# Optimization experiments

Measured on AMD Instinct MI355X. Metric: run time of the kernel, lower is better.

## Reference

```python
import jax, jax.numpy as jnp
import numpy as np

H = 1024   # lstm hidden size
F = 512    # feature dim
P = 66     # pose dim
T_IN = 10
T_OUT = 25


def _glorot(key, shape):
    fan = shape[-1]
    return jax.random.normal(key, shape, dtype=jnp.float32) / np.sqrt(fan)


def setup_inputs() -> dict:
    key = jax.random.key(0)
    ks = jax.random.split(key, 24)
    B = 256
    inp = {
        'x': jax.random.normal(ks[0], (B, T_IN, P), dtype=jnp.float32),
        'z': jax.random.normal(ks[1], (B, T_IN, P), dtype=jnp.float32),
        'for_resid': jax.random.normal(ks[2], (B, T_OUT, P), dtype=jnp.float32),
        # ToFeature: Linear(66 -> 512)
        'tf_w': _glorot(ks[3], (F, P)), 'tf_b': jnp.zeros((F,), jnp.float32),
        # encoder LSTM(512 -> 1024)
        'enc_wih': _glorot(ks[4], (4 * H, F)), 'enc_whh': _glorot(ks[5], (4 * H, H)),
        'enc_bih': jnp.zeros((4 * H,), jnp.float32), 'enc_bhh': jnp.zeros((4 * H,), jnp.float32),
        # encoder_post LSTM(512 -> 1024)
        'encp_wih': _glorot(ks[6], (4 * H, F)), 'encp_whh': _glorot(ks[7], (4 * H, H)),
        'encp_bih': jnp.zeros((4 * H,), jnp.float32), 'encp_bhh': jnp.zeros((4 * H,), jnp.float32),
        # decoder cell LSTM(512 -> 1024)
        'dec_wih': _glorot(ks[8], (4 * H, F)), 'dec_whh': _glorot(ks[9], (4 * H, H)),
        'dec_bih': jnp.zeros((4 * H,), jnp.float32), 'dec_bhh': jnp.zeros((4 * H,), jnp.float32),
        # decoder lin: Linear(1024 -> 512)
        'lin_w': _glorot(ks[10], (F, H)), 'lin_b': jnp.zeros((F,), jnp.float32),
        # ToPose: Linear(1024 -> 66)
        'tp_w': _glorot(ks[11], (P, H)), 'tp_b': jnp.zeros((P,), jnp.float32),
    }
    return inp


def _lstm_step(h, c, xt, wih, whh, bih, bhh):
    gates = xt @ wih.T + bih + h @ whh.T + bhh  # (B, 4H)
    i, f, g, o = jnp.split(gates, 4, axis=-1)
    c_new = jax.nn.sigmoid(f) * c + jax.nn.sigmoid(i) * jnp.tanh(g)
    h_new = jax.nn.sigmoid(o) * jnp.tanh(c_new)
    return h_new, c_new


def _lstm_scan(xs, wih, whh, bih, bhh):
    # xs: (T, B, I)
    B = xs.shape[1]
    h0 = jnp.zeros((B, H), xs.dtype)
    c0 = jnp.zeros((B, H), xs.dtype)

    def step(carry, xt):
        h, c = carry
        h, c = _lstm_step(h, c, xt, wih, whh, bih, bhh)
        return (h, c), h

    (h_n, c_n), all_h = jax.lax.scan(step, (h0, c0), xs)
    return all_h, h_n, c_n


def reference(x, z, for_resid, tf_w, tf_b,
              enc_wih, enc_whh, enc_bih, enc_bhh,
              encp_wih, encp_whh, encp_bih, encp_bhh,
              dec_wih, dec_whh, dec_bih, dec_bhh,
              lin_w, lin_b, tp_w, tp_b):
    # ToFeature + permute to time-major (T, B, F)
    xf = jnp.transpose(x @ tf_w.T + tf_b, (1, 0, 2))
    zf = jnp.transpose(z @ tf_w.T + tf_b, (1, 0, 2))

    all_h, h_n, c_n = _lstm_scan(xf, enc_wih, enc_whh, enc_bih, enc_bhh)   # (10,B,H)
    all_hz, _, _ = _lstm_scan(zf, encp_wih, encp_whh, encp_bih, encp_bhh)  # (10,B,H)

    def dec_step(carry, _):
        h, c = carry                                   # (B,H), (B,H)
        cat_h = jnp.concatenate([all_h, h[None], all_hz], axis=0)  # (21,B,H)
        scores = jnp.einsum('bh,tbh->tb', c, cat_h)
        attw = jax.nn.softmax(scores, axis=0)
        atth = jnp.einsum('tb,tbh->bh', attw, cat_h)   # attention context -> LSTM h0
        inp = h @ lin_w.T + lin_b                      # (B,F)
        h_new, c_new = _lstm_step(atth, c, inp, dec_wih, dec_whh, dec_bih, dec_bhh)
        return (h_new, c_new), h_new

    _, dec_hs = jax.lax.scan(dec_step, (h_n, c_n), None, length=T_OUT)  # (25,B,H)
    out = jnp.transpose(dec_hs, (1, 0, 2))             # (B,25,H)
    o = out @ tp_w.T + tp_b                            # (B,25,66)
    return o + for_resid
```

## Files before the change

### kernel.cpp

```cpp
#include <hip/hip_runtime.h>
#include <hip/hip_bf16.h>
#include <hip/hip_cooperative_groups.h>

namespace cg = cooperative_groups;

#define DEV __device__ __forceinline__

typedef unsigned short u16;
typedef short bf16x8_t __attribute__((ext_vector_type(8)));
typedef float f32x4_t __attribute__((ext_vector_type(4)));

constexpr int NBLK = 256;
constexpr int NTHR = 512;
constexpr int NT_ALL = NBLK * NTHR;
constexpr size_t HSTRIDE = 256 * 1024;
constexpr int SMEM_BYTES = 98304;

struct Params {
  const float *x, *z, *resid, *tf_w, *tf_b;
  const float *e_wih, *e_whh, *e_bih, *e_bhh;
  const float *p_wih, *p_whh, *p_bih, *p_bhh;
  const float *d_wih, *d_whh, *d_bih, *d_bhh;
  const float *lin_w, *lin_b, *tp_w, *tp_b;
  u16 *Wenc, *Wencp, *Wdec, *wihP, *linT, *tpw;
  float *bias_e, *bias_ep, *bias_d, *bias_part;
  u16 *xf, *zf;
  u16 *he, *hp;
  u16 *hs;
  u16 *atth;
  float *c_pub;
  unsigned long long *px;
  unsigned *flag1;
  unsigned *bar;
  float *out;
};

DEV float b2f(u16 v) { unsigned u = ((unsigned)v) << 16; float f; __builtin_memcpy(&f, &u, 4); return f; }
DEV u16 f2b(float f) {
  unsigned u; __builtin_memcpy(&u, &f, 4);
  unsigned r = u + 0x7fffu + ((u >> 16) & 1u);
  return (u16)(r >> 16);
}
DEV unsigned pk2(float a, float b) { return (unsigned)f2b(a) | ((unsigned)f2b(b) << 16); }
DEV uint4 cvt8(const float* s) {
  float4 a = *(const float4*)s;
  float4 b = *(const float4*)(s + 4);
  uint4 r;
  r.x = pk2(a.x, a.y); r.y = pk2(a.z, a.w);
  r.z = pk2(b.x, b.y); r.w = pk2(b.z, b.w);
  return r;
}
DEV float sigm(float x) { return 1.0f / (1.0f + __expf(-x)); }
DEV f32x4_t fzero4() { f32x4_t v = {0.f, 0.f, 0.f, 0.f}; return v; }

DEV void gll16(const void* g, void* l) {
  __builtin_amdgcn_global_load_lds(
      (const __attribute__((address_space(1))) void*)g,
      (__attribute__((address_space(3))) void*)l, 16, 0, 0);
}

template <typename T> DEV void st_wt(T* p, T v) {
  __hip_atomic_store(p, v, __ATOMIC_RELAXED, __HIP_MEMORY_SCOPE_AGENT);
}
template <typename T> DEV T ld_byp(const T* p) {
  return __hip_atomic_load(p, __ATOMIC_RELAXED, __HIP_MEMORY_SCOPE_AGENT);
}

DEV void fullbar(unsigned* ctrs, int myidx, unsigned tgt, int tid) {
  asm volatile("s_waitcnt vmcnt(0)" ::: "memory");
  __syncthreads();
  if (tid == 0) atomicAdd(&ctrs[myidx * 16], 1u);
  if (tid < 8) { while (ld_byp(&ctrs[tid * 16]) < tgt) __builtin_amdgcn_s_sleep(2); }
  __syncthreads();
}
DEV void gbar(unsigned* ctrs, int cbase, int myidx, unsigned tgt, int tid) {
  asm volatile("s_waitcnt vmcnt(0)" ::: "memory");
  __syncthreads();
  if (tid == 0) atomicAdd(&ctrs[(cbase + myidx) * 16], 1u);
  if (tid < 4) { while (ld_byp(&ctrs[(cbase + tid) * 16]) < tgt) __builtin_amdgcn_s_sleep(2); }
  __syncthreads();
}
DEV void lanebar(unsigned* ctrs, int cbase, unsigned tgt, int j, int tid) {
  asm volatile("s_waitcnt vmcnt(0)" ::: "memory");
  __syncthreads();
  if (tid == 0) atomicAdd(&ctrs[(cbase + (j & 1)) * 16], 1u);
  if (tid < 2) { while (ld_byp(&ctrs[(cbase + tid) * 16]) < tgt) __builtin_amdgcn_s_sleep(2); }
  __syncthreads();
}

template <int PM>
DEV void gemm64(const u16* __restrict__ xa, int ldx, int xcols,
                const u16* __restrict__ ha, int ldh,
                const u16* __restrict__ wsrc, int ldw, int K,
                int m0, int n0, int tid, char* sm, f32x4_t acc[4]) {
  char* lA = sm;
  char* lB = sm + 32768;
  const int NK = K >> 6;
  const int row = tid >> 3;
  const int usw = ((tid & 7) ^ (row & 7)) * 8;
  const int wv = tid >> 6;
  char* laD = lA + (wv << 10);
  char* lbD = lB + (wv << 10);
  const u16* aX = xa + (size_t)(m0 + row) * ldx + usw;
  const u16* aH = ha + (size_t)(m0 + row) * ldh + usw - xcols;
  const u16* bW0 = wsrc + (size_t)(n0 + row) * ldw + usw;
  const u16* bW1 = bW0 + (size_t)64 * ldw;

  auto sA = [&](int ks) {
    const int k0 = ks << 6;
    const u16* g = (k0 < xcols) ? (aX + k0) : (aH + k0);
    gll16(g, laD + (((ks + 2) & 3) << 13));
  };
  auto sB = [&](int ks) {
    const int k0 = ks << 6;
    const int so = ((ks + 2) & 3) << 14;
    gll16(bW0 + k0, lbD + so);
    gll16(bW1 + k0, lbD + so + 8192);
  };

  const int l = tid & 63, l15 = l & 15, lhi = l >> 4;
  const int wr = wv >> 2, wc = wv & 3;
  const int rA0 = wr * 32 + l15, rA1 = rA0 + 16;
  const int nB0 = wc * 32 + l15, nB1 = nB0 + 16;
  const int a00 = rA0 * 128 + ((lhi ^ (rA0 & 7)) << 4);
  const int a01 = rA0 * 128 + (((lhi + 4) ^ (rA0 & 7)) << 4);
  const int a10 = rA1 * 128 + ((lhi ^ (rA1 & 7)) << 4);
  const int a11 = rA1 * 128 + (((lhi + 4) ^ (rA1 & 7)) << 4);
  const int b00 = nB0 * 128 + ((lhi ^ (nB0 & 7)) << 4);
  const int b01 = nB0 * 128 + (((lhi + 4) ^ (nB0 & 7)) << 4);
  const int b10 = nB1 * 128 + ((lhi ^ (nB1 & 7)) << 4);
  const int b11 = nB1 * 128 + (((lhi + 4) ^ (nB1 & 7)) << 4);

  if (PM == 0) { sA(0); sB(0); sA(1); sB(1); }
  if (PM == 2) { sA(0); sA(1); }

#pragma unroll 1
  for (int ks = 0; ks < NK; ++ks) {
    if (ks + 2 < NK) { sA(ks + 2); sB(ks + 2); }
    if (PM == 2 && ks == 0)  asm volatile("s_waitcnt vmcnt(4)" ::: "memory");
    else if (ks + 2 < NK)    asm volatile("s_waitcnt vmcnt(6)" ::: "memory");
    else if (ks + 2 == NK)   asm volatile("s_waitcnt vmcnt(3)" ::: "memory");
    else                     asm volatile("s_waitcnt vmcnt(0)" ::: "memory");
    __builtin_amdgcn_s_barrier();
    const char* A  = lA + (((ks + 2) & 3) << 13);
    const char* Bq = lB + (((ks + 2) & 3) << 14);
#pragma unroll
    for (int kh = 0; kh < 2; ++kh) {
      bf16x8_t va0 = *(const bf16x8_t*)(A + (kh ? a01 : a00));
      bf16x8_t va1 = *(const bf16x8_t*)(A + (kh ? a11 : a10));
      bf16x8_t vb0 = *(const bf16x8_t*)(Bq + (kh ? b01 : b00));
      bf16x8_t vb1 = *(const bf16x8_t*)(Bq + (kh ? b11 : b10));
      acc[0] = __builtin_amdgcn_mfma_f32_16x16x32_bf16(va0, vb0, acc[0], 0, 0, 0);
      acc[1] = __builtin_amdgcn_mfma_f32_16x16x32_bf16(va0, vb1, acc[1], 0, 0, 0);
      acc[2] = __builtin_amdgcn_mfma_f32_16x16x32_bf16(va1, vb0, acc[2], 0, 0, 0);
      acc[3] = __builtin_amdgcn_mfma_f32_16x16x32_bf16(va1, vb1, acc[3], 0, 0, 0);
    }
  }
  asm volatile("s_waitcnt lgkmcnt(0)" ::: "memory");
  __builtin_amdgcn_s_barrier();
}

DEV void preA(const u16* src, int lds_, int m0, int tid, char* sm, int ks) {
  const int row = tid >> 3, usw = ((tid & 7) ^ (row & 7)) * 8, wv = tid >> 6;
  gll16(src + (size_t)(m0 + row) * lds_ + (ks << 6) + usw,
        sm + (wv << 10) + (((ks + 2) & 3) << 13));
}
DEV void preB(const u16* w, int ldw, int n0, int tid, char* sm, int ks) {
  const int row = tid >> 3, usw = ((tid & 7) ^ (row & 7)) * 8, wv = tid >> 6;
  char* d = sm + 32768 + (wv << 10) + (((ks + 2) & 3) << 14);
  gll16(w + (size_t)(n0 + row) * ldw + (ks << 6) + usw, d);
  gll16(w + (size_t)(n0 + 64 + row) * ldw + (ks << 6) + usw, d + 8192);
}

DEV void lstm_ep(const f32x4_t acc[4], int tid, char* sm,
                 const float* __restrict__ bias, float cc[4],
                 const float* __restrict__ cinit,
                 u16* __restrict__ hw, float* __restrict__ cpub,
                 int m0, int n0) {
  float* gl = (float*)sm;
  const int l = tid & 63, l15 = l & 15, lhi = l >> 4;
  const int wv = tid >> 6, wr = wv >> 2, wc = wv & 3;
#pragma unroll
  for (int mf = 0; mf < 2; ++mf)
#pragma unroll
    for (int nf = 0; nf < 2; ++nf)
#pragma unroll
      for (int qq = 0; qq < 4; ++qq)
        gl[(wr * 32 + mf * 16 + lhi * 4 + qq) * 128 + wc * 32 + nf * 16 + l15] =
            acc[mf * 2 + nf][qq];
  __syncthreads();
#pragma unroll
  for (int it = 0; it < 4; ++it) {
    int idx = it * 512 + tid;
    int r = idx >> 5, jj = idx & 31;
    f32x4_t g4 = *(const f32x4_t*)(gl + r * 128 + jj * 4);
    f32x4_t b4 = *(const f32x4_t*)(bias + n0 + jj * 4);
    float ig = sigm(g4[0] + b4[0]);
    float fg = sigm(g4[1] + b4[1]);
    float g_ = tanhf(g4[2] + b4[2]);
    float og = sigm(g4[3] + b4[3]);
    size_t off = (size_t)(m0 + r) * 1024 + (n0 >> 2) + jj;
    float cold = cinit ? ld_byp(cinit + off) : cc[it];
    float cn = fg * cold + ig * g_;
    cc[it] = cn;
    float hn = og * tanhf(cn);
    st_wt(&hw[off], f2b(hn));
    if (cpub) st_wt(&cpub[off], cn);
  }
  __syncthreads();
}

DEV void wx_store(const f32x4_t acc[4], int tid, u16* __restrict__ Wdec,
                  int m0, int n0) {
  const int l = tid & 63, l15 = l & 15, lhi = l >> 4;
  const int wv = tid >> 6, wr = wv >> 2, wc = wv & 3;
#pragma unroll
  for (int mf = 0; mf < 2; ++mf)
#pragma unroll
    for (int nf = 0; nf < 2; ++nf)
#pragma unroll
      for (int qq = 0; qq < 4; ++qq) {
        int r = m0 + wr * 32 + mf * 16 + lhi * 4 + qq;
        int c = n0 + wc * 32 + nf * 16 + l15;
        st_wt(&Wdec[(size_t)r * 2048 + c], f2b(acc[mf * 2 + nf][qq]));
      }
}

DEV void px_store(const f32x4_t acc[4], int tid, unsigned long long* base) {
#pragma unroll
  for (int i = 0; i < 8; ++i) {
    float lo = acc[i >> 1][(i & 1) * 2 + 0];
    float hi = acc[i >> 1][(i & 1) * 2 + 1];
    unsigned a_, b_; __builtin_memcpy(&a_, &lo, 4); __builtin_memcpy(&b_, &hi, 4);
    st_wt(base + (size_t)i * 512 + tid,
          (unsigned long long)a_ | ((unsigned long long)b_ << 32));
  }
}
DEV void px_merge(f32x4_t acc[4], int tid, const unsigned long long* base) {
#pragma unroll
  for (int i = 0; i < 8; ++i) {
    unsigned long long u = ld_byp(base + (size_t)i * 512 + tid);
    unsigned a_ = (unsigned)u, b_ = (unsigned)(u >> 32);
    float lo, hi; __builtin_memcpy(&lo, &a_, 4); __builtin_memcpy(&hi, &b_, 4);
    acc[i >> 1][(i & 1) * 2 + 0] += lo;
    acc[i >> 1][(i & 1) * 2 + 1] += hi;
  }
}

DEV void phase0_tf(const Params& p, int bid, int tid, char* sm) {
  float* xs = (float*)sm;
  float* zs = (float*)(sm + 2688);
  for (int g = tid; g < 660; g += NTHR) {
    int t = g / 66, qd = g - t * 66;
    xs[g] = p.x[((size_t)bid * 10 + t) * 66 + qd];
    zs[g] = p.z[((size_t)bid * 10 + t) * 66 + qd];
  }
  __syncthreads();
  const int n = tid;
  float accx[10], accz[10];
  float bn = p.tf_b[n];
#pragma unroll
  for (int t = 0; t < 10; ++t) { accx[t] = bn; accz[t] = bn; }
  const float* wrow = p.tf_w + (size_t)n * 66;
  for (int k = 0; k < 66; ++k) {
    float wk = wrow[k];
#pragma unroll
    for (int t = 0; t < 10; ++t) {
      accx[t] = fmaf(wk, xs[t * 66 + k], accx[t]);
      accz[t] = fmaf(wk, zs[t * 66 + k], accz[t]);
    }
  }
#pragma unroll
  for (int t = 0; t < 10; ++t) {
    p.xf[(size_t)t * 131072 + (size_t)bid * 512 + n] = f2b(accx[t]);
    p.zf[(size_t)t * 131072 + (size_t)bid * 512 + n] = f2b(accz[t]);
  }
  __syncthreads();
}

DEV void phase0a(const Params& p, int gtid) {
  for (int g = gtid; g < 786432; g += NT_ALL) {
    int row = g / 192;
    int u = g - row * 192;
    int k = u * 8;
    int nsrc = (row & 3) * 1024 + (row >> 2);
    const float* s1 = (k < 512) ? (p.e_wih + (size_t)nsrc * 512 + k)
                                : (p.e_whh + (size_t)nsrc * 1024 + (k - 512));
    ((uint4*)p.Wenc)[g] = cvt8(s1);
    const float* s2 = (k < 512) ? (p.p_wih + (size_t)nsrc * 512 + k)
                                : (p.p_whh + (size_t)nsrc * 1024 + (k - 512));
    ((uint4*)p.Wencp)[g] = cvt8(s2);
  }
  for (int g = gtid; g < 524288; g += NT_ALL) {
    int row = g >> 7, u = g & 127;
    int nsrc = (row & 3) * 1024 + (row >> 2);
    ((uint4*)p.Wdec)[row * 256 + 128 + u] = cvt8(p.d_whh + (size_t)nsrc * 1024 + u * 8);
  }
  for (int g = gtid; g < 262144; g += NT_ALL) {
    int row = g >> 6, u = g & 63;
    int nsrc = (row & 3) * 1024 + (row >> 2);
    ((uint4*)p.wihP)[g] = cvt8(p.d_wih + (size_t)nsrc * 512 + u * 8);
  }
  for (int g = gtid; g < 524288; g += NT_ALL) {
    int f = g >> 10, h = g & 1023;
    p.linT[(size_t)h * 512 + f] = f2b(p.lin_w[g]);
  }
  for (int g = gtid; g < 8448; g += NT_ALL)
    ((uint4*)p.tpw)[g] = cvt8(p.tp_w + g * 8);
  for (int g = gtid; g < 4096; g += NT_ALL) {
    int nsrc = (g & 3) * 1024 + (g >> 2);
    p.bias_e[g]  = p.e_bih[nsrc] + p.e_bhh[nsrc];
    p.bias_ep[g] = p.p_bih[nsrc] + p.p_bhh[nsrc];
  }
  for (int g = gtid; g < 32768; g += NT_ALL) {
    int cell = g >> 3, sub = g & 7;
    int nsrc = (cell & 3) * 1024 + (cell >> 2);
    const float* wr_ = p.d_wih + (size_t)nsrc * 512 + sub * 64;
    const float* lb = p.lin_b + sub * 64;
    float s = 0.f;
    for (int f = 0; f < 64; ++f) s += wr_[f] * lb[f];
    p.bias_part[g] = s;
  }
  uint4 zz; zz.x = zz.y = zz.z = zz.w = 0u;
  for (int g = gtid; g < 32768; g += NT_ALL) { ((uint4*)p.he)[g] = zz; ((uint4*)p.hp)[g] = zz; }
}

DEV void attention(const Params& p, const u16* hd_prev, const float* cpub,
                   u16* atth_s, int b, int tid, char* sm) {
  u16*   catl = (u16*)sm;
  float* cl   = (float*)(sm + 43008);
  float* sc   = (float*)(sm + 47104);
  for (int g = tid; g < 2688; g += NTHR) {
    int t = g >> 7, hu = g & 127;
    const u16* src;
    if (t < 10)       src = p.he + (size_t)(t + 1) * HSTRIDE;
    else if (t == 10) src = hd_prev;
    else              src = p.hp + (size_t)(t - 10) * HSTRIDE;
    ((uint4*)catl)[g] = *(const uint4*)(src + (size_t)b * 1024 + hu * 8);
  }
  for (int g = tid; g < 512; g += NTHR) {
    unsigned long long v = ld_byp(((const unsigned long long*)(cpub + (size_t)b * 1024)) + g);
    ((unsigned long long*)cl)[g] = v;
  }
  __syncthreads();
  const int wv = tid >> 6, l = tid & 63;
  for (int t = wv; t < 21; t += 8) {
    float s = 0.f;
    const u16* cr = catl + t * 1024;
    for (int hh = l; hh < 1024; hh += 64) s += cl[hh] * b2f(cr[hh]);
#pragma unroll
    for (int o = 32; o; o >>= 1) s += __shfl_down(s, o);
    if (l == 0) sc[t] = s;
  }
  __syncthreads();
  float m = -1e30f;
#pragma unroll
  for (int t = 0; t < 21; ++t) m = fmaxf(m, sc[t]);
  float e[21]; float den = 0.f;
#pragma unroll
  for (int t = 0; t < 21; ++t) { e[t] = __expf(sc[t] - m); den += e[t]; }
  float inv = 1.0f / den;
  const int h0 = tid * 2;
  float a0 = 0.f, a1 = 0.f;
#pragma unroll
  for (int t = 0; t < 21; ++t) {
    float w_ = e[t] * inv;
    unsigned v = *(const unsigned*)(catl + t * 1024 + h0);
    a0 += w_ * b2f((u16)(v & 0xffff));
    a1 += w_ * b2f((u16)(v >> 16));
  }
  st_wt(((unsigned*)(atth_s + (size_t)b * 1024)) + tid, pk2(a0, a1));
  __syncthreads();
}

DEV void finalproj(const Params& p, int b, int tid, char* sm) {
  u16* hl = (u16*)sm;
  for (int g = tid; g < 3200; g += NTHR) {
    int t = g >> 7, hu = g & 127;
    ((uint4*)hl)[g] = *(const uint4*)(p.hs + ((size_t)(t * 256 + b)) * 1024 + hu * 8);
  }
  __syncthreads();
  if (tid < 330) {
    int pcol = tid % 66, tg = tid / 66;
    float acc[5] = {0.f, 0.f, 0.f, 0.f, 0.f};
    const u16* wrow = p.tpw + (size_t)pcol * 1024;
    for (int hc = 0; hc < 128; ++hc) {
      uint4 wv4 = ((const uint4*)wrow)[hc];
      float wf[8];
      wf[0] = b2f(wv4.x & 0xffff); wf[1] = b2f(wv4.x >> 16);
      wf[2] = b2f(wv4.y & 0xffff); wf[3] = b2f(wv4.y >> 16);
      wf[4] = b2f(wv4.z & 0xffff); wf[5] = b2f(wv4.z >> 16);
      wf[6] = b2f(wv4.w & 0xffff); wf[7] = b2f(wv4.w >> 16);
#pragma unroll
      for (int r = 0; r < 5; ++r) {
        int t = tg * 5 + r;
        uint4 hv = ((const uint4*)(hl + t * 1024))[hc];
        float s;
        s  = wf[0] * b2f(hv.x & 0xffff) + wf[1] * b2f(hv.x >> 16);
        s += wf[2] * b2f(hv.y & 0xffff) + wf[3] * b2f(hv.y >> 16);
        s += wf[4] * b2f(hv.z & 0xffff) + wf[5] * b2f(hv.z >> 16);
        s += wf[6] * b2f(hv.w & 0xffff) + wf[7] * b2f(hv.w >> 16);
        acc[r] += s;
      }
    }
    float bb = p.tp_b[pcol];
#pragma unroll
    for (int r = 0; r < 5; ++r) {
      int t = tg * 5 + r;
      size_t o = (size_t)b * 1650 + (size_t)t * 66 + pcol;
      p.out[o] = acc[r] + bb + p.resid[o];
    }
  }
}

__global__ __launch_bounds__(NTHR) void model_kernel(Params p) {
  cg::grid_group gg = cg::this_grid();
  extern __shared__ __align__(16) char sm[];
  const int tid = threadIdx.x;
  const int bid = blockIdx.x;
  const int gtid = bid * NTHR + tid;

  phase0_tf(p, bid, tid, sm);
  phase0a(p, gtid);
  if (bid == 0) {
    if (tid < 24)  st_wt(&p.bar[tid * 16], 0u);
    if (tid < 128) st_wt(&p.flag1[tid * 16], 0u);
  }
  gg.sync();

  for (int g = gtid; g < 4096; g += NT_ALL) {
    int nsrc = (g & 3) * 1024 + (g >> 2);
    float s = p.d_bih[nsrc] + p.d_bhh[nsrc];
#pragma unroll
    for (int k8 = 0; k8 < 8; ++k8) s += p.bias_part[g * 8 + k8];
    st_wt(&p.bias_d[g], s);
  }
#pragma unroll 1
  for (int i = 0; i < 2; ++i) {
    int tt = bid * 2 + i;
    int m0w = (tt & 63) << 6;
    int n0w = (tt >> 6) << 7;
    f32x4_t acc[4] = {fzero4(), fzero4(), fzero4(), fzero4()};
    gemm64<0>(p.wihP, 512, 512, p.wihP, 512, p.linT, 512, 512, m0w, n0w, tid, sm, acc);
    wx_store(acc, tid, p.Wdec, m0w, n0w);
  }

  const int grp = bid >> 7;
  const int q = bid & 127;
  const int m0 = (q >> 5) << 6;
  const int n0 = (q & 31) << 7;
  const int cb = grp ? 12 : 8;
  const int cidx = q >> 5;

  const int lane = bid >> 6, j = bid & 63;
  const int m0d = lane << 6;
  const int role = j >> 5, jj = j & 31;
  const int n0d = jj << 7;
  const int tixd = lane * 32 + jj;

  const u16* xsrc = grp ? p.zf : p.xf;
  const u16* Wg   = grp ? p.Wencp : p.Wenc;
  u16* hbuf       = grp ? p.hp : p.he;
  const float* bias_g = grp ? p.bias_ep : p.bias_e;

  preA(xsrc, 512, m0, tid, sm, 0);
  preB(Wg, 1536, n0, tid, sm, 0);
  preA(xsrc, 512, m0, tid, sm, 1);
  preB(Wg, 1536, n0, tid, sm, 1);
  fullbar(p.bar, bid & 7, 1u * 32, tid);

  float cc[4] = {0.f, 0.f, 0.f, 0.f};

#pragma unroll 1
  for (int t = 0; t < 10; ++t) {
    f32x4_t acc[4] = {fzero4(), fzero4(), fzero4(), fzero4()};
    gemm64<1>(xsrc + (size_t)t * 131072, 512, 512, hbuf + (size_t)t * HSTRIDE, 1024,
              Wg, 1536, 1536, m0, n0, tid, sm, acc);
    lstm_ep(acc, tid, sm, bias_g, cc, (const float*)0,
            hbuf + (size_t)(t + 1) * HSTRIDE,
            (!grp && t == 9) ? p.c_pub : (float*)0, m0, n0);
    if (t < 9) {
      preA(xsrc + (size_t)(t + 1) * 131072, 512, m0, tid, sm, 0);
      preB(Wg, 1536, n0, tid, sm, 0);
      preA(xsrc + (size_t)(t + 1) * 131072, 512, m0, tid, sm, 1);
      preB(Wg, 1536, n0, tid, sm, 1);
    } else {
      const u16* wd = role ? (p.Wdec + 1024) : p.Wdec;
      preB(wd, 2048, n0d, tid, sm, 0);
      preB(wd, 2048, n0d, tid, sm, 1);
    }
    gbar(p.bar, cb, cidx, (unsigned)(t + 1) * 32, tid);
  }
  fullbar(p.bar, bid & 7, 2u * 32, tid);

  float cd[4] = {0.f, 0.f, 0.f, 0.f};
  unsigned long long* px0 = p.px + (size_t)tixd * 4096;
  unsigned long long* px1 = p.px + (size_t)(128 + tixd) * 4096;
#pragma unroll 1
  for (int s = 0; s < 25; ++s) {
    const u16* hd_prev = (s == 0) ? (p.he + (size_t)10 * HSTRIDE)
                                  : (p.hs + (size_t)(s - 1) * HSTRIDE);
    u16* atth_s = p.atth + (size_t)s * HSTRIDE;
    attention(p, hd_prev, p.c_pub + (size_t)(s & 1) * 262144, atth_s, bid, tid, sm);
    lanebar(p.bar, 16 + lane * 2, (unsigned)(2 * s + 1) * 32, j, tid);
    f32x4_t acc[4] = {fzero4(), fzero4(), fzero4(), fzero4()};
    unsigned long long* pxs = (s & 1) ? px1 : px0;
    if (role == 0) {
      gemm64<2>(hd_prev, 1024, 1024, hd_prev, 1024, p.Wdec, 2048, 1024,
                m0d, n0d, tid, sm, acc);
      px_store(acc, tid, pxs);
      asm volatile("s_waitcnt vmcnt(0)" ::: "memory");
      __syncthreads();
      if (tid == 0) st_wt(&p.flag1[tixd * 16], (unsigned)(s + 1));
      preB(p.Wdec, 2048, n0d, tid, sm, 0);
      preB(p.Wdec, 2048, n0d, tid, sm, 1);
    } else {
      gemm64<2>(atth_s, 1024, 1024, atth_s, 1024, p.Wdec + 1024, 2048, 1024,
                m0d, n0d, tid, sm, acc);
      if (tid == 0) {
        while (ld_byp(&p.flag1[tixd * 16]) < (unsigned)(s + 1)) __builtin_amdgcn_s_sleep(2);
      }
      __syncthreads();
      px_merge(acc, tid, pxs);
      lstm_ep(acc, tid, sm, p.bias_d, cd,
              (s == 0) ? p.c_pub : (const float*)0,
              p.hs + (size_t)s * HSTRIDE,
              p.c_pub + (size_t)((s + 1) & 1) * 262144, m0d, n0d);
      preB(p.Wdec + 1024, 2048, n0d, tid, sm, 0);
      preB(p.Wdec + 1024, 2048, n0d, tid, sm, 1);
    }
    lanebar(p.bar, 16 + lane * 2, (unsigned)(2 * s + 2) * 32, j, tid);
  }

  finalproj(p, bid, tid, sm);
}

extern "C" void kernel_launch(void* const* d_in, const int* in_sizes, int n_in,
                              void* d_out, int out_size, void* d_ws, size_t ws_size,
                              hipStream_t stream) {
  (void)in_sizes; (void)n_in; (void)out_size;
  Params P;
  P.x     = (const float*)d_in[0];
  P.z     = (const float*)d_in[1];
  P.resid = (const float*)d_in[2];
  P.tf_w  = (const float*)d_in[3];
  P.tf_b  = (const float*)d_in[4];
  P.e_wih = (const float*)d_in[5];
  P.e_whh = (const float*)d_in[6];
  P.e_bih = (const float*)d_in[7];
  P.e_bhh = (const float*)d_in[8];
  P.p_wih = (const float*)d_in[9];
  P.p_whh = (const float*)d_in[10];
  P.p_bih = (const float*)d_in[11];
  P.p_bhh = (const float*)d_in[12];
  P.d_wih = (const float*)d_in[13];
  P.d_whh = (const float*)d_in[14];
  P.d_bih = (const float*)d_in[15];
  P.d_bhh = (const float*)d_in[16];
  P.lin_w = (const float*)d_in[17];
  P.lin_b = (const float*)d_in[18];
  P.tp_w  = (const float*)d_in[19];
  P.tp_b  = (const float*)d_in[20];

  char* w = (char*)d_ws;
  size_t o = 0;
  auto take = [&](size_t bytes) { char* r = w + o; o = (o + bytes + 255) & ~(size_t)255; return r; };
  P.Wenc  = (u16*)take(4096ull * 1536 * 2);
  P.Wencp = (u16*)take(4096ull * 1536 * 2);
  P.Wdec  = (u16*)take(4096ull * 2048 * 2);
  P.wihP  = (u16*)take(4096ull * 512 * 2);
  P.linT  = (u16*)take(1024ull * 512 * 2);
  P.tpw   = (u16*)take(66ull * 1024 * 2);
  P.bias_e    = (float*)take(4096 * 4);
  P.bias_ep   = (float*)take(4096 * 4);
  P.bias_d    = (float*)take(4096 * 4);
  P.bias_part = (float*)take(32768 * 4);
  P.xf  = (u16*)take(10ull * 256 * 512 * 2);
  P.zf  = (u16*)take(10ull * 256 * 512 * 2);
  P.he  = (u16*)take(11ull * 256 * 1024 * 2);
  P.hp  = (u16*)take(11ull * 256 * 1024 * 2);
  P.hs  = (u16*)take(25ull * 256 * 1024 * 2);
  P.atth = (u16*)take(25ull * 256 * 1024 * 2);
  P.c_pub = (float*)take(2ull * 256 * 1024 * 4);
  P.px    = (unsigned long long*)take(2ull * 128 * 4096 * 8);
  P.flag1 = (unsigned*)take(128 * 64);
  P.bar   = (unsigned*)take(24 * 64);
  P.out = (float*)d_out;

  if (o > ws_size) return;

  hipFuncSetAttribute((const void*)model_kernel,
                      hipFuncAttributeMaxDynamicSharedMemorySize, SMEM_BYTES);

  void* args[] = { &P };
  hipLaunchCooperativeKernel((const void*)model_kernel, dim3(NBLK, 1, 1),
                             dim3(NTHR, 1, 1), args, SMEM_BYTES, stream);
}
```

Before: 905.8 us.

## Split decoder GEMM by N tiles instead of K halves, removing partial-sum exchange

Each decoder block used to compute half of the K reduction (h part or attention part) and swap partial sums through global memory with a flag handshake. Now each block computes a 64x64 output tile over the full K, running the h-part GEMM before the lane barrier and the attention part after it. This removes the px store/merge traffic and the flag spin-wait, and overlaps the h-part GEMM with waiting for attention. In exchange tiles are smaller (less MFMA reuse per load), lane barriers now count 8 counters instead of 2, and the attention shared-memory buffers are moved to avoid the new staging area.

```diff
diff --git a/kernel.cpp b/kernel.cpp
--- a/kernel.cpp
+++ b/kernel.cpp
@@ -29,8 +29,6 @@
   u16 *hs;
   u16 *atth;
   float *c_pub;
-  unsigned long long *px;
-  unsigned *flag1;
   unsigned *bar;
   float *out;
 };
@@ -66,10 +64,10 @@
   return __hip_atomic_load(p, __ATOMIC_RELAXED, __HIP_MEMORY_SCOPE_AGENT);
 }
 
-DEV void fullbar(unsigned* ctrs, int myidx, unsigned tgt, int tid) {
+DEV void fullbar(unsigned* ctrs, int bid, unsigned tgt, int tid) {
   asm volatile("s_waitcnt vmcnt(0)" ::: "memory");
   __syncthreads();
-  if (tid == 0) atomicAdd(&ctrs[myidx * 16], 1u);
+  if (tid == 0) atomicAdd(&ctrs[(bid & 7) * 16], 1u);
   if (tid < 8) { while (ld_byp(&ctrs[tid * 16]) < tgt) __builtin_amdgcn_s_sleep(2); }
   __syncthreads();
 }
@@ -80,19 +78,19 @@
   if (tid < 4) { while (ld_byp(&ctrs[(cbase + tid) * 16]) < tgt) __builtin_amdgcn_s_sleep(2); }
   __syncthreads();
 }
-DEV void lanebar(unsigned* ctrs, int cbase, unsigned tgt, int j, int tid) {
+DEV void lanebar8(unsigned* ctrs, int lane, int j, unsigned tgt, int tid) {
   asm volatile("s_waitcnt vmcnt(0)" ::: "memory");
   __syncthreads();
-  if (tid == 0) atomicAdd(&ctrs[(cbase + (j & 1)) * 16], 1u);
-  if (tid < 2) { while (ld_byp(&ctrs[(cbase + tid) * 16]) < tgt) __builtin_amdgcn_s_sleep(2); }
+  if (tid == 0) atomicAdd(&ctrs[(16 + lane * 8 + (j & 7)) * 16], 1u);
+  if (tid < 8) { while (ld_byp(&ctrs[(16 + lane * 8 + tid) * 16]) < tgt) __builtin_amdgcn_s_sleep(1); }
   __syncthreads();
 }
 
 template <int PM>
-DEV void gemm64(const u16* __restrict__ xa, int ldx, int xcols,
-                const u16* __restrict__ ha, int ldh,
-                const u16* __restrict__ wsrc, int ldw, int K,
-                int m0, int n0, int tid, char* sm, f32x4_t acc[4]) {
+DEV void gemm128(const u16* __restrict__ xa, int ldx, int xcols,
+                 const u16* __restrict__ ha, int ldh,
+                 const u16* __restrict__ wsrc, int ldw, int K,
+                 int m0, int n0, int tid, char* sm, f32x4_t acc[4]) {
   char* lA = sm;
   char* lB = sm + 32768;
   const int NK = K >> 6;
@@ -132,15 +130,13 @@
   const int b11 = nB1 * 128 + (((lhi + 4) ^ (nB1 & 7)) << 4);
 
   if (PM == 0) { sA(0); sB(0); sA(1); sB(1); }
-  if (PM == 2) { sA(0); sA(1); }
 
 #pragma unroll 1
   for (int ks = 0; ks < NK; ++ks) {
     if (ks + 2 < NK) { sA(ks + 2); sB(ks + 2); }
-    if (PM == 2 && ks == 0)  asm volatile("s_waitcnt vmcnt(4)" ::: "memory");
-    else if (ks + 2 < NK)    asm volatile("s_waitcnt vmcnt(6)" ::: "memory");
-    else if (ks + 2 == NK)   asm volatile("s_waitcnt vmcnt(3)" ::: "memory");
-    else                     asm volatile("s_waitcnt vmcnt(0)" ::: "memory");
+    if (ks + 2 < NK)        asm volatile("s_waitcnt vmcnt(6)" ::: "memory");
+    else if (ks + 2 == NK)  asm volatile("s_waitcnt vmcnt(3)" ::: "memory");
+    else                    asm volatile("s_waitcnt vmcnt(0)" ::: "memory");
     __builtin_amdgcn_s_barrier();
     const char* A  = lA + (((ks + 2) & 3) << 13);
     const char* Bq = lB + (((ks + 2) & 3) << 14);
@@ -160,23 +156,86 @@
   __builtin_amdgcn_s_barrier();
 }
 
-DEV void preA(const u16* src, int lds_, int m0, int tid, char* sm, int ks) {
+DEV void preA128(const u16* src, int lds_, int m0, int tid, char* sm, int ks) {
   const int row = tid >> 3, usw = ((tid & 7) ^ (row & 7)) * 8, wv = tid >> 6;
   gll16(src + (size_t)(m0 + row) * lds_ + (ks << 6) + usw,
         sm + (wv << 10) + (((ks + 2) & 3) << 13));
 }
-DEV void preB(const u16* w, int ldw, int n0, int tid, char* sm, int ks) {
+DEV void preB128(const u16* w, int ldw, int n0, int tid, char* sm, int ks) {
   const int row = tid >> 3, usw = ((tid & 7) ^ (row & 7)) * 8, wv = tid >> 6;
   char* d = sm + 32768 + (wv << 10) + (((ks + 2) & 3) << 14);
   gll16(w + (size_t)(n0 + row) * ldw + (ks << 6) + usw, d);
   gll16(w + (size_t)(n0 + 64 + row) * ldw + (ks << 6) + usw, d + 8192);
 }
 
-DEV void lstm_ep(const f32x4_t acc[4], int tid, char* sm,
-                 const float* __restrict__ bias, float cc[4],
-                 const float* __restrict__ cinit,
-                 u16* __restrict__ hw, float* __restrict__ cpub,
-                 int m0, int n0) {
+DEV void gemm64d(const u16* __restrict__ a, int lda,
+                 const u16* __restrict__ w, int ldw, int K,
+                 int m0, int n0, int tid, char* sm, f32x4_t acc[2]) {
+  char* lB = sm;
+  char* lA = sm + 32768;
+  const int NK = K >> 6;
+  const int row = tid >> 3, uu = tid & 7;
+  const int usw = uu ^ (row & 7);
+  const int wv = tid >> 6;
+  char* la_base = lA + (wv << 10);
+  char* lb_base = lB + (wv << 10);
+  const u16* aS = a + (size_t)(m0 + row) * lda + usw * 8;
+  const u16* bS = w + (size_t)(n0 + row) * ldw + usw * 8;
+
+  auto stageA = [&](int ks) { gll16(aS + (ks << 6), la_base + ((ks & 3) << 13)); };
+  auto stage  = [&](int ks) {
+    gll16(aS + (ks << 6), la_base + ((ks & 3) << 13));
+    gll16(bS + (ks << 6), lb_base + ((ks & 3) << 13));
+  };
+
+  const int l = tid & 63, l15 = l & 15, lhi = l >> 4;
+  const int wr = wv >> 1, wc = wv & 1;
+  const int rA = wr * 16 + l15;
+  const int aoff0 = rA * 128 + ((lhi ^ (rA & 7)) << 4);
+  const int aoff1 = rA * 128 + (((lhi + 4) ^ (rA & 7)) << 4);
+  const int nB0 = wc * 32 + l15, nB1 = nB0 + 16;
+  const int boff00 = nB0 * 128 + ((lhi ^ (nB0 & 7)) << 4);
+  const int boff01 = nB0 * 128 + (((lhi + 4) ^ (nB0 & 7)) << 4);
+  const int boff10 = nB1 * 128 + ((lhi ^ (nB1 & 7)) << 4);
+  const int boff11 = nB1 * 128 + (((lhi + 4) ^ (nB1 & 7)) << 4);
+
+  stageA(0); stageA(1);
+
+#pragma unroll 1
+  for (int ks = 0; ks < NK; ++ks) {
+    if (ks + 2 < NK) stage(ks + 2);
+    if (ks == 0)            asm volatile("s_waitcnt vmcnt(3)" ::: "memory");
+    else if (ks + 2 < NK)   asm volatile("s_waitcnt vmcnt(4)" ::: "memory");
+    else if (ks + 2 == NK)  asm volatile("s_waitcnt vmcnt(2)" ::: "memory");
+    else                    asm volatile("s_waitcnt vmcnt(0)" ::: "memory");
+    __builtin_amdgcn_s_barrier();
+    const char* A  = lA + ((ks & 3) << 13);
+    const char* Bb = lB + ((ks & 3) << 13);
+    bf16x8_t a0  = *(const bf16x8_t*)(A + aoff0);
+    bf16x8_t a1  = *(const bf16x8_t*)(A + aoff1);
+    bf16x8_t b00 = *(const bf16x8_t*)(Bb + boff00);
+    bf16x8_t b01 = *(const bf16x8_t*)(Bb + boff01);
+    bf16x8_t b10 = *(const bf16x8_t*)(Bb + boff10);
+    bf16x8_t b11 = *(const bf16x8_t*)(Bb + boff11);
+    acc[0] = __builtin_amdgcn_mfma_f32_16x16x32_bf16(a0, b00, acc[0], 0, 0, 0);
+    acc[0] = __builtin_amdgcn_mfma_f32_16x16x32_bf16(a1, b01, acc[0], 0, 0, 0);
+    acc[1] = __builtin_amdgcn_mfma_f32_16x16x32_bf16(a0, b10, acc[1], 0, 0, 0);
+    acc[1] = __builtin_amdgcn_mfma_f32_16x16x32_bf16(a1, b11, acc[1], 0, 0, 0);
+  }
+  asm volatile("s_waitcnt lgkmcnt(0)" ::: "memory");
+  __builtin_amdgcn_s_barrier();
+}
+
+DEV void preB64(const u16* w, int ldw, int n0, int tid, char* sm, int ks) {
+  const int row = tid >> 3, usw = (tid & 7) ^ (row & 7), wv = tid >> 6;
+  gll16(w + (size_t)(n0 + row) * ldw + (ks << 6) + usw * 8,
+        sm + (wv << 10) + ((ks & 3) << 13));
+}
+
+DEV void lstm_ep128(const f32x4_t acc[4], int tid, char* sm,
+                    const float* __restrict__ bias, float cc[4],
+                    u16* __restrict__ hw, float* __restrict__ cpub,
+                    int m0, int n0) {
   float* gl = (float*)sm;
   const int l = tid & 63, l15 = l & 15, lhi = l >> 4;
   const int wv = tid >> 6, wr = wv >> 2, wc = wv & 3;
@@ -194,6 +253,40 @@
     int idx = it * 512 + tid;
     int r = idx >> 5, jj = idx & 31;
     f32x4_t g4 = *(const f32x4_t*)(gl + r * 128 + jj * 4);
+    f32x4_t b4 = *(const f32x4_t*)(bias + n0 + jj * 4);
+    float ig = sigm(g4[0] + b4[0]);
+    float fg = sigm(g4[1] + b4[1]);
+    float g_ = tanhf(g4[2] + b4[2]);
+    float og = sigm(g4[3] + b4[3]);
+    float cn = fg * cc[it] + ig * g_;
+    cc[it] = cn;
+    float hn = og * tanhf(cn);
+    size_t off = (size_t)(m0 + r) * 1024 + (n0 >> 2) + jj;
+    st_wt(&hw[off], f2b(hn));
+    if (cpub) st_wt(&cpub[off], cn);
+  }
+  __syncthreads();
+}
+
+DEV void lstm_ep64(const f32x4_t acc[2], int tid, char* sm,
+                   const float* __restrict__ bias, float cc[2],
+                   const float* __restrict__ cinit,
+                   u16* __restrict__ hw, float* __restrict__ cpub,
+                   int m0, int n0) {
+  float* gl = (float*)(sm + 49152);
+  const int l = tid & 63, l15 = l & 15, lhi = l >> 4;
+  const int wv = tid >> 6, wr = wv >> 1, wc = wv & 1;
+#pragma unroll
+  for (int jf = 0; jf < 2; ++jf)
+#pragma unroll
+    for (int qq = 0; qq < 4; ++qq)
+      gl[(wr * 16 + lhi * 4 + qq) * 64 + wc * 32 + jf * 16 + l15] = acc[jf][qq];
+  __syncthreads();
+#pragma unroll
+  for (int it = 0; it < 2; ++it) {
+    int idx = it * 512 + tid;
+    int r = idx >> 4, jj = idx & 15;
+    f32x4_t g4 = *(const f32x4_t*)(gl + r * 64 + jj * 4);
     f32x4_t b4 = *(const f32x4_t*)(bias + n0 + jj * 4);
     float ig = sigm(g4[0] + b4[0]);
     float fg = sigm(g4[1] + b4[1]);
@@ -226,27 +319,6 @@
       }
 }
 
-DEV void px_store(const f32x4_t acc[4], int tid, unsigned long long* base) {
-#pragma unroll
-  for (int i = 0; i < 8; ++i) {
-    float lo = acc[i >> 1][(i & 1) * 2 + 0];
-    float hi = acc[i >> 1][(i & 1) * 2 + 1];
-    unsigned a_, b_; __builtin_memcpy(&a_, &lo, 4); __builtin_memcpy(&b_, &hi, 4);
-    st_wt(base + (size_t)i * 512 + tid,
-          (unsigned long long)a_ | ((unsigned long long)b_ << 32));
-  }
-}
-DEV void px_merge(f32x4_t acc[4], int tid, const unsigned long long* base) {
-#pragma unroll
-  for (int i = 0; i < 8; ++i) {
-    unsigned long long u = ld_byp(base + (size_t)i * 512 + tid);
-    unsigned a_ = (unsigned)u, b_ = (unsigned)(u >> 32);
-    float lo, hi; __builtin_memcpy(&lo, &a_, 4); __builtin_memcpy(&hi, &b_, 4);
-    acc[i >> 1][(i & 1) * 2 + 0] += lo;
-    acc[i >> 1][(i & 1) * 2 + 1] += hi;
-  }
-}
-
 DEV void phase0_tf(const Params& p, int bid, int tid, char* sm) {
   float* xs = (float*)sm;
   float* zs = (float*)(sm + 2688);
@@ -327,9 +399,9 @@
 
 DEV void attention(const Params& p, const u16* hd_prev, const float* cpub,
                    u16* atth_s, int b, int tid, char* sm) {
-  u16*   catl = (u16*)sm;
-  float* cl   = (float*)(sm + 43008);
-  float* sc   = (float*)(sm + 47104);
+  u16*   catl = (u16*)(sm + 16384);
+  float* cl   = (float*)(sm + 59392);
+  float* sc   = (float*)(sm + 63488);
   for (int g = tid; g < 2688; g += NTHR) {
     int t = g >> 7, hu = g & 127;
     const u16* src;
@@ -422,10 +494,7 @@
 
   phase0_tf(p, bid, tid, sm);
   phase0a(p, gtid);
-  if (bid == 0) {
-    if (tid < 24)  st_wt(&p.bar[tid * 16], 0u);
-    if (tid < 128) st_wt(&p.flag1[tid * 16], 0u);
-  }
+  if (bid == 0 && tid < 48) st_wt(&p.bar[tid * 16], 0u);
   gg.sync();
 
   for (int g = gtid; g < 4096; g += NT_ALL) {
@@ -435,101 +504,85 @@
     for (int k8 = 0; k8 < 8; ++k8) s += p.bias_part[g * 8 + k8];
     st_wt(&p.bias_d[g], s);
   }
+
 #pragma unroll 1
   for (int i = 0; i < 2; ++i) {
     int tt = bid * 2 + i;
     int m0w = (tt & 63) << 6;
     int n0w = (tt >> 6) << 7;
     f32x4_t acc[4] = {fzero4(), fzero4(), fzero4(), fzero4()};
-    gemm64<0>(p.wihP, 512, 512, p.wihP, 512, p.linT, 512, 512, m0w, n0w, tid, sm, acc);
+    gemm128<0>(p.wihP, 512, 512, p.wihP, 512, p.linT, 512, 512,
+               m0w, n0w, tid, sm, acc);
     wx_store(acc, tid, p.Wdec, m0w, n0w);
   }
 
   const int grp = bid >> 7;
   const int q = bid & 127;
-  const int m0 = (q >> 5) << 6;
-  const int n0 = (q & 31) << 7;
+  const int m0e = (q >> 5) << 6;
+  const int n0e = (q & 31) << 7;
   const int cb = grp ? 12 : 8;
   const int cidx = q >> 5;
 
   const int lane = bid >> 6, j = bid & 63;
   const int m0d = lane << 6;
-  const int role = j >> 5, jj = j & 31;
-  const int n0d = jj << 7;
-  const int tixd = lane * 32 + jj;
+  const int n0d = ((j & 7) * 8 + (j >> 3)) << 6;
 
   const u16* xsrc = grp ? p.zf : p.xf;
   const u16* Wg   = grp ? p.Wencp : p.Wenc;
   u16* hbuf       = grp ? p.hp : p.he;
   const float* bias_g = grp ? p.bias_ep : p.bias_e;
 
-  preA(xsrc, 512, m0, tid, sm, 0);
-  preB(Wg, 1536, n0, tid, sm, 0);
-  preA(xsrc, 512, m0, tid, sm, 1);
-  preB(Wg, 1536, n0, tid, sm, 1);
-  fullbar(p.bar, bid & 7, 1u * 32, tid);
+  preA128(xsrc, 512, m0e, tid, sm, 0);
+  preB128(Wg, 1536, n0e, tid, sm, 0);
+  preA128(xsrc, 512, m0e, tid, sm, 1);
+  preB128(Wg, 1536, n0e, tid, sm, 1);
+  fullbar(p.bar, bid, 32u, tid);
 
   float cc[4] = {0.f, 0.f, 0.f, 0.f};
 
 #pragma unroll 1
   for (int t = 0; t < 10; ++t) {
     f32x4_t acc[4] = {fzero4(), fzero4(), fzero4(), fzero4()};
-    gemm64<1>(xsrc + (size_t)t * 131072, 512, 512, hbuf + (size_t)t * HSTRIDE, 1024,
-              Wg, 1536, 1536, m0, n0, tid, sm, acc);
-    lstm_ep(acc, tid, sm, bias_g, cc, (const float*)0,
-            hbuf + (size_t)(t + 1) * HSTRIDE,
-            (!grp && t == 9) ? p.c_pub : (float*)0, m0, n0);
+    gemm128<1>(xsrc + (size_t)t * 131072, 512, 512, hbuf + (size_t)t * HSTRIDE, 1024,
+               Wg, 1536, 1536, m0e, n0e, tid, sm, acc);
+    lstm_ep128(acc, tid, sm, bias_g, cc, hbuf + (size_t)(t + 1) * HSTRIDE,
+               (!grp && t == 9) ? p.c_pub : (float*)0, m0e, n0e);
     if (t < 9) {
-      preA(xsrc + (size_t)(t + 1) * 131072, 512, m0, tid, sm, 0);
-      preB(Wg, 1536, n0, tid, sm, 0);
-      preA(xsrc + (size_t)(t + 1) * 131072, 512, m0, tid, sm, 1);
-      preB(Wg, 1536, n0, tid, sm, 1);
+      preA128(xsrc + (size_t)(t + 1) * 131072, 512, m0e, tid, sm, 0);
+      preB128(Wg, 1536, n0e, tid, sm, 0);
+      preA128(xsrc + (size_t)(t + 1) * 131072, 512, m0e, tid, sm, 1);
+      preB128(Wg, 1536, n0e, tid, sm, 1);
     } else {
-      const u16* wd = role ? (p.Wdec + 1024) : p.Wdec;
-      preB(wd, 2048, n0d, tid, sm, 0);
-      preB(wd, 2048, n0d, tid, sm, 1);
+      preB64(p.Wdec, 2048, n0d, tid, sm, 0);
+      preB64(p.Wdec, 2048, n0d, tid, sm, 1);
     }
     gbar(p.bar, cb, cidx, (unsigned)(t + 1) * 32, tid);
   }
-  fullbar(p.bar, bid & 7, 2u * 32, tid);
-
-  float cd[4] = {0.f, 0.f, 0.f, 0.f};
-  unsigned long long* px0 = p.px + (size_t)tixd * 4096;
-  unsigned long long* px1 = p.px + (size_t)(128 + tixd) * 4096;
+  fullbar(p.bar, bid, 64u, tid);
+
+  float cd[2] = {0.f, 0.f};
+  unsigned lep = 0;
 #pragma unroll 1
   for (int s = 0; s < 25; ++s) {
     const u16* hd_prev = (s == 0) ? (p.he + (size_t)10 * HSTRIDE)
                                   : (p.hs + (size_t)(s - 1) * HSTRIDE);
     u16* atth_s = p.atth + (size_t)s * HSTRIDE;
     attention(p, hd_prev, p.c_pub + (size_t)(s & 1) * 262144, atth_s, bid, tid, sm);
-    lanebar(p.bar, 16 + lane * 2, (unsigned)(2 * s + 1) * 32, j, tid);
-    f32x4_t acc[4] = {fzero4(), fzero4(), fzero4(), fzero4()};
-    unsigned long long* pxs = (s & 1) ? px1 : px0;
-    if (role == 0) {
-      gemm64<2>(hd_prev, 1024, 1024, hd_prev, 1024, p.Wdec, 2048, 1024,
-                m0d, n0d, tid, sm, acc);
-      px_store(acc, tid, pxs);
-      asm volatile("s_waitcnt vmcnt(0)" ::: "memory");
-      __syncthreads();
-      if (tid == 0) st_wt(&p.flag1[tixd * 16], (unsigned)(s + 1));
-      preB(p.Wdec, 2048, n0d, tid, sm, 0);
-      preB(p.Wdec, 2048, n0d, tid, sm, 1);
-    } else {
-      gemm64<2>(atth_s, 1024, 1024, atth_s, 1024, p.Wdec + 1024, 2048, 1024,
-                m0d, n0d, tid, sm, acc);
-      if (tid == 0) {
-        while (ld_byp(&p.flag1[tixd * 16]) < (unsigned)(s + 1)) __builtin_amdgcn_s_sleep(2);
-      }
-      __syncthreads();
-      px_merge(acc, tid, pxs);
-      lstm_ep(acc, tid, sm, p.bias_d, cd,
+    f32x4_t acc[2]; acc[0] = fzero4(); acc[1] = fzero4();
+    gemm64d(hd_prev, 1024, p.Wdec, 2048, 1024, m0d, n0d, tid, sm, acc);
+    preB64(p.Wdec + 1024, 2048, n0d, tid, sm, 0);
+    preB64(p.Wdec + 1024, 2048, n0d, tid, sm, 1);
+    ++lep; lanebar8(p.bar, lane, j, lep * 8u, tid);
+    gemm64d(atth_s, 1024, p.Wdec + 1024, 2048, 1024, m0d, n0d, tid, sm, acc);
+    lstm_ep64(acc, tid, sm, p.bias_d, cd,
               (s == 0) ? p.c_pub : (const float*)0,
               p.hs + (size_t)s * HSTRIDE,
               p.c_pub + (size_t)((s + 1) & 1) * 262144, m0d, n0d);
-      preB(p.Wdec + 1024, 2048, n0d, tid, sm, 0);
-      preB(p.Wdec + 1024, 2048, n0d, tid, sm, 1);
+    if (s < 24) {
+      preB64(p.Wdec, 2048, n0d, tid, sm, 0);
+      preB64(p.Wdec, 2048, n0d, tid, sm, 1);
     }
-    lanebar(p.bar, 16 + lane * 2, (unsigned)(2 * s + 2) * 32, j, tid);
+    ++lep; lanebar8(p.bar, lane, j, lep * 8u, tid);
   }
 
   finalproj(p, bid, tid, sm);
@@ -582,9 +635,7 @@
   P.hs  = (u16*)take(25ull * 256 * 1024 * 2);
   P.atth = (u16*)take(25ull * 256 * 1024 * 2);
   P.c_pub = (float*)take(2ull * 256 * 1024 * 4);
-  P.px    = (unsigned long long*)take(2ull * 128 * 4096 * 8);
-  P.flag1 = (unsigned*)take(128 * 64);
-  P.bar   = (unsigned*)take(24 * 64);
+  P.bar   = (unsigned*)take(48 * 64);
   P.out = (float*)d_out;
 
   if (o > ws_size) return;
```

Result: faster. 840.5 us (-7.2%).
